# Optimization experiments

Hardware: AMD Instinct MI355X
Metric: run time of the kernel (lower is better)

Reference implementation:

```python
import jax, jax.numpy as jnp
from jax import lax
import numpy as np
from functools import reduce

# --- module hyperparameters (init_kwargs defaults) ---
T_LOW = 0.5; T_HIGH = 0.9; SIGMAS = (1.0, 2.0); BETA = 0.5
Z_RADIUS = 1; XY_RADIUS = 0; DUST_MIN_SIZE = 100; EPS = 1e-7
MAX_HYST_ITERS = 256   # flood-fill iteration cap (converges far earlier on real data)
MAX_CC_ITERS = 256     # label-propagation iteration cap


def _gauss_kernel(sigma):
    # separable gaussian, truncate at 3 sigma (standard scipy convention)
    r = int(3.0 * sigma + 0.5)
    x = np.arange(-r, r + 1, dtype=np.float32)
    k = np.exp(-(x * x) / (2.0 * sigma * sigma))
    return jnp.asarray(k / k.sum())


def _conv1d_axis(v, k, axis):
    # 'same' zero-padded 1D correlation along `axis` of a 3D volume
    r = k.shape[0] // 2
    pad = [(0, 0)] * 3; pad[axis] = (r, r)
    vp = jnp.pad(v, pad)
    n = v.shape[axis]
    out = jnp.zeros_like(v)
    for i in range(k.shape[0]):  # tiny fixed tap loop, vectorized over the volume
        sl = [slice(None)] * 3; sl[axis] = slice(i, i + n)
        out = out + k[i] * vp[tuple(sl)]
    return out


def _shifts6(x, pad_val):
    # 6-connected neighbor views (cross connectivity, matches ndi default)
    p = jnp.pad(x, 1, constant_values=pad_val)
    c = slice(1, -1)
    return (p[:-2, c, c], p[2:, c, c], p[c, :-2, c], p[c, 2:, c], p[c, c, :-2], p[c, c, 2:])


def _axis_morph(m, axis, radius, dilate):
    # box dilation/erosion along one axis (box SE is separable)
    op = jnp.logical_or if dilate else jnp.logical_and
    pad_val = (not dilate)
    for _ in range(radius):
        pad = [(1, 1) if a == axis else (0, 0) for a in range(3)]
        p = jnp.pad(m, pad, constant_values=pad_val)
        lo = tuple(slice(0, -2) if a == axis else slice(None) for a in range(3))
        hi = tuple(slice(2, None) if a == axis else slice(None) for a in range(3))
        m = op(op(m, p[lo]), p[hi])
    return m


def _hysteresis(vol):
    # keep low-threshold voxels connected to a high-threshold voxel (flood fill)
    low = vol > T_LOW
    high = vol > T_HIGH
    def body(st):
        m, _, i = st
        nm = m
        for s in _shifts6(m, False):
            nm = nm | s
        nm = nm & low
        return nm, jnp.any(nm != m), i + 1
    mask, _, _ = lax.while_loop(lambda st: st[1] & (st[2] < MAX_HYST_ITERS), body,
                                (high, jnp.bool_(True), jnp.int32(0)))
    return mask


def _closing(mask):
    # anisotropic binary closing with box SE (2*z_r+1, 2*xy_r+1, 2*xy_r+1)
    for axis, r in ((0, Z_RADIUS), (1, XY_RADIUS), (2, XY_RADIUS)):
        mask = _axis_morph(mask, axis, r, dilate=True)
    for axis, r in ((0, Z_RADIUS), (1, XY_RADIUS), (2, XY_RADIUS)):
        mask = _axis_morph(mask, axis, r, dilate=False)
    return mask


def _remove_small(mask):
    # connected-component labeling via max-label propagation, then size filter
    n = mask.size
    idx = jnp.arange(1, n + 1, dtype=jnp.int32).reshape(mask.shape)
    lab0 = jnp.where(mask, idx, 0)
    def body(st):
        l, _, i = st
        nl = l
        for s in _shifts6(l, 0):
            nl = jnp.maximum(nl, s)
        nl = jnp.where(mask, nl, 0)
        return nl, jnp.any(nl != l), i + 1
    lab, _, _ = lax.while_loop(lambda st: st[1] & (st[2] < MAX_CC_ITERS), body,
                               (lab0, jnp.bool_(True), jnp.int32(0)))
    counts = jax.ops.segment_sum(mask.ravel().astype(jnp.int32), lab.ravel(), num_segments=n + 1)
    return mask & (counts[lab] >= DUST_MIN_SIZE)


def _process_volume(v):
    d2 = jnp.asarray([1.0, -2.0, 1.0], v.dtype)
    surfs = []
    for sigma in SIGMAS:
        k = _gauss_kernel(sigma)
        s = v
        for ax in range(3):
            s = _conv1d_axis(s, k, ax)
        scale = sigma * sigma
        fxx = _conv1d_axis(s, d2, 0) * scale
        fyy = _conv1d_axis(s, d2, 1) * scale
        fzz = _conv1d_axis(s, d2, 2) * scale
        surf = jnp.exp(-(fxx * fxx + fyy * fyy) / (BETA * BETA * (fzz * fzz + EPS))) * jnp.abs(fzz)
        mx = surf.max()
        surfs.append(jnp.where(mx > 0, surf / (mx + EPS), jnp.zeros_like(surf)))
    surfaceness = reduce(jnp.maximum, surfs)  # max over sigma stack
    vol = lax.stop_gradient(v * surfaceness)  # binarization pipeline is piecewise constant
    mask = _hysteresis(vol)
    mask = _closing(mask)
    if DUST_MIN_SIZE > 0:
        mask = _remove_small(mask)
    return mask.astype(v.dtype)


def setup_inputs() -> dict:
    key = jax.random.key(0)
    outputs = jax.random.uniform(key, (2, 192, 192, 192), dtype=jnp.float32)
    return {"outputs": outputs}


def reference(outputs):
    return jax.vmap(_process_volume)(outputs)
```

## Files before the change

kernel.cpp:

```cpp
#include <hip/hip_runtime.h>
#include <cmath>

#define D3   192
#define SZP  (D3*D3)
#define NVOX (D3*D3*D3)
#define NTOT (2*NVOX)
#define NBLK (NTOT/256)
#define W3   (NTOT/64)
#define WBLK (W3/256)
#define NSUM (W3/64)
#define NQ   (NTOT/4)
#define NQB  (NQ/256)
#define BPB  (NVOX/256)

#define HT 16
#define HH 8
#define HL (HT+2*HH)
#define HLDS (HL*HL*3)
#define NHT  (12*12*2)

typedef unsigned long long u64;

struct Taps13 { float k[13]; };

__device__ __forceinline__ void coords(int idx, int& x, int& y, int& z, int& b) {
  x = idx % D3;
  y = (idx / D3) % D3;
  z = (idx / SZP) % D3;
  b = idx / NVOX;
}

template<int AXIS, int R>
__global__ void __launch_bounds__(256) conv1d_k(const float* __restrict__ in,
                                                float* __restrict__ out, Taps13 t) {
  int idx = blockIdx.x * 256 + threadIdx.x;
  int x, y, z, b; coords(idx, x, y, z, b);
  int c = (AXIS == 0) ? z : (AXIS == 1) ? y : x;
  const int stride = (AXIS == 0) ? SZP : (AXIS == 1) ? D3 : 1;
  float acc = 0.f;
#pragma unroll
  for (int i = -R; i <= R; ++i) {
    int cc = c + i;
    if (cc >= 0 && cc < D3)
      acc = __fadd_rn(acc, __fmul_rn(t.k[i + R], in[idx + i * stride]));
  }
  out[idx] = acc;
}

__global__ void __launch_bounds__(256) surf_k(const float* __restrict__ s,
                                              float* __restrict__ surf,
                                              float* __restrict__ bmax,
                                              float scale) {
  int idx = blockIdx.x * 256 + threadIdx.x;
  int x, y, z, b; coords(idx, x, y, z, b);
  float ctr = s[idx];
  float fxx, fyy, fzz;
  { float acc = 0.f;
    if (z > 0)      acc = __fadd_rn(acc, __fmul_rn(1.f, s[idx - SZP]));
    acc = __fadd_rn(acc, __fmul_rn(-2.f, ctr));
    if (z < D3 - 1) acc = __fadd_rn(acc, __fmul_rn(1.f, s[idx + SZP]));
    fxx = __fmul_rn(acc, scale); }
  { float acc = 0.f;
    if (y > 0)      acc = __fadd_rn(acc, __fmul_rn(1.f, s[idx - D3]));
    acc = __fadd_rn(acc, __fmul_rn(-2.f, ctr));
    if (y < D3 - 1) acc = __fadd_rn(acc, __fmul_rn(1.f, s[idx + D3]));
    fyy = __fmul_rn(acc, scale); }
  { float acc = 0.f;
    if (x > 0)      acc = __fadd_rn(acc, __fmul_rn(1.f, s[idx - 1]));
    acc = __fadd_rn(acc, __fmul_rn(-2.f, ctr));
    if (x < D3 - 1) acc = __fadd_rn(acc, __fmul_rn(1.f, s[idx + 1]));
    fzz = __fmul_rn(acc, scale); }

  float num = __fadd_rn(__fmul_rn(fxx, fxx), __fmul_rn(fyy, fyy));
  float den = __fmul_rn(0.25f, __fadd_rn(__fmul_rn(fzz, fzz), 1e-7f));
  float arg = __fdiv_rn(-num, den);
  float sv  = __fmul_rn(expf(arg), fabsf(fzz));
  surf[idx] = sv;

  float m = sv;
  #pragma unroll
  for (int off = 32; off > 0; off >>= 1) m = fmaxf(m, __shfl_down(m, off));
  __shared__ float wred[4];
  int lane = threadIdx.x & 63, wid = threadIdx.x >> 6;
  if (lane == 0) wred[wid] = m;
  __syncthreads();
  if (threadIdx.x == 0)
    bmax[blockIdx.x] = fmaxf(fmaxf(wred[0], wred[1]), fmaxf(wred[2], wred[3]));
}

__global__ void __launch_bounds__(256) reduce_max_k(const float* __restrict__ bmax,
                                                    unsigned int* __restrict__ mxp) {
  int b = blockIdx.x;
  const float* p = bmax + b * BPB;
  float m = 0.f;
  for (int i = threadIdx.x; i < BPB; i += 256) m = fmaxf(m, p[i]);
  #pragma unroll
  for (int off = 32; off > 0; off >>= 1) m = fmaxf(m, __shfl_down(m, off));
  __shared__ float wred[4];
  int lane = threadIdx.x & 63, wid = threadIdx.x >> 6;
  if (lane == 0) wred[wid] = m;
  __syncthreads();
  if (threadIdx.x == 0)
    mxp[b] = __float_as_uint(fmaxf(fmaxf(wred[0], wred[1]), fmaxf(wred[2], wred[3])));
}

__global__ void __launch_bounds__(256) mask_init_pack_k(const float* __restrict__ v,
                                                        const float* __restrict__ s1,
                                                        const float* __restrict__ s2,
                                                        const unsigned int* __restrict__ mx,
                                                        u64* __restrict__ lowW,
                                                        u64* __restrict__ mW) {
  int idx = blockIdx.x * 256 + threadIdx.x;
  int b = idx / NVOX;
  float m1 = __uint_as_float(mx[b]);
  float m2 = __uint_as_float(mx[2 + b]);
  float n1 = (m1 > 0.f) ? __fdiv_rn(s1[idx], __fadd_rn(m1, 1e-7f)) : 0.f;
  float n2 = (m2 > 0.f) ? __fdiv_rn(s2[idx], __fadd_rn(m2, 1e-7f)) : 0.f;
  float vol = __fmul_rn(v[idx], fmaxf(n1, n2));
  u64 bl = __ballot(vol > 0.5f);
  u64 bh = __ballot(vol > 0.9f);
  if ((threadIdx.x & 63) == 0) {
    lowW[idx >> 6] = bl;
    mW[idx >> 6]   = bh;
  }
}

__global__ void __launch_bounds__(256) hyst8_k(const u64* __restrict__ src,
                                               u64* __restrict__ dst,
                                               const u64* __restrict__ lowW,
                                               const int* __restrict__ fprev,
                                               int* __restrict__ fcur,
                                               int* __restrict__ chg, int iter) {
  if (iter > 0 && chg[iter - 1] == 0) return;
  const int r = blockIdx.x + 12 * blockIdx.y + 144 * blockIdx.z;
  if (iter > 0) {
    bool act = false;
    for (int dz = -1; dz <= 1 && !act; ++dz) {
      int zz = (int)blockIdx.y + dz; if (zz < 0 || zz >= 12) continue;
      for (int dy = -1; dy <= 1; ++dy) {
        int yy = (int)blockIdx.x + dy; if (yy < 0 || yy >= 12) continue;
        if (fprev[yy + 12 * zz + 144 * blockIdx.z]) { act = true; break; }
      }
    }
    if (!act) { if (threadIdx.x == 0) fcur[r] = 0; return; }
  }

  __shared__ u64 sA[HLDS], sB[HLDS];
  __shared__ int blkC;
  const int t = threadIdx.x;
  if (t == 0) blkC = 0;
  const int y0 = blockIdx.x * HT - HH;
  const int z0 = blockIdx.y * HT - HH;
  const int b  = blockIdx.z;

  u64 lowr[4][3], orig[4][3];
#pragma unroll
  for (int j = 0; j < 4; ++j) {
    int l = t + 256 * j;
    int yy = l & 31, zz = l >> 5;
    int y = y0 + yy, z = z0 + zz;
    bool in = (y >= 0 && y < D3 && z >= 0 && z < D3);
    int wb = 3 * y + 576 * z + 110592 * b;
#pragma unroll
    for (int xw = 0; xw < 3; ++xw) {
      u64 sv = in ? src[wb + xw]  : 0ull;
      u64 lv = in ? lowW[wb + xw] : 0ull;
      sA[l * 3 + xw] = sv;
      orig[j][xw] = sv;
      lowr[j][xw] = lv;
    }
  }
  __syncthreads();

  u64* cur = sA; u64* nxt = sB;
  for (int s = 0; s < 8; ++s) {
#pragma unroll
    for (int j = 0; j < 4; ++j) {
      int l = t + 256 * j;
      int yy = l & 31, zz = l >> 5;
      int base = l * 3;
      u64 w0 = cur[base], w1 = cur[base + 1], w2 = cur[base + 2];
      u64 n0 = w0 | (w0 << 1) | (w0 >> 1) | (w1 << 63);
      u64 n1 = w1 | (w1 << 1) | (w1 >> 1) | (w0 >> 63) | (w2 << 63);
      u64 n2 = w2 | (w2 << 1) | (w2 >> 1) | (w1 >> 63);
      if (yy > 0)  { n0 |= cur[base - 3];  n1 |= cur[base - 2];  n2 |= cur[base - 1]; }
      if (yy < 31) { n0 |= cur[base + 3];  n1 |= cur[base + 4];  n2 |= cur[base + 5]; }
      if (zz > 0)  { n0 |= cur[base - 96]; n1 |= cur[base - 95]; n2 |= cur[base - 94]; }
      if (zz < 31) { n0 |= cur[base + 96]; n1 |= cur[base + 97]; n2 |= cur[base + 98]; }
      nxt[base]     = n0 & lowr[j][0];
      nxt[base + 1] = n1 & lowr[j][1];
      nxt[base + 2] = n2 & lowr[j][2];
    }
    __syncthreads();
    u64* tmp = cur; cur = nxt; nxt = tmp;
  }

  bool ch = false;
#pragma unroll
  for (int j = 0; j < 4; ++j) {
    int l = t + 256 * j;
    int yy = l & 31, zz = l >> 5;
    if (yy >= HH && yy < HH + HT && zz >= HH && zz < HH + HT) {
      int y = y0 + yy, z = z0 + zz;
      int wb = 3 * y + 576 * z + 110592 * b;
#pragma unroll
      for (int xw = 0; xw < 3; ++xw) {
        u64 o = cur[l * 3 + xw];
        ch |= (o != orig[j][xw]);
        dst[wb + xw] = o;
      }
    }
  }
  if (ch) blkC = 1;
  __syncthreads();
  if (t == 0) { fcur[r] = blkC; if (blkC) chg[iter] = 1; }
}

__global__ void __launch_bounds__(256) close_z_k(const u64* __restrict__ mi,
                                                 u64* __restrict__ mo) {
  int w = blockIdx.x * 256 + threadIdx.x;
  int z = (w / 576) % D3;
  u64 c   = mi[w];
  u64 zm1 = (z > 0)      ? mi[w - 576]  : 0ull;
  u64 zm2 = (z > 1)      ? mi[w - 1152] : 0ull;
  u64 zp1 = (z < D3 - 1) ? mi[w + 576]  : 0ull;
  u64 zp2 = (z < D3 - 2) ? mi[w + 1152] : 0ull;
  u64 d0 = c | zm1 | zp1;
  u64 e  = d0;
  if (z > 0)      e &= (zm2 | zm1 | c);
  if (z < D3 - 1) e &= (c | zp1 | zp2);
  mo[w] = e;
}

__global__ void __launch_bounds__(256) label_init_k(const u64* __restrict__ closedW,
                                                    int* __restrict__ lab) {
  int idx = blockIdx.x * 256 + threadIdx.x;
  int bit = (int)((closedW[idx >> 6] >> (idx & 63)) & 1ull);
  lab[idx] = bit ? (idx % NVOX) + 1 : 0;
}

__device__ __forceinline__ int imax2(int a, int b) { return a > b ? a : b; }

__global__ void __launch_bounds__(256) cc_word_k(const int* __restrict__ src,
                                                 int* __restrict__ dst,
                                                 const u64* __restrict__ chgPrev,
                                                 u64* __restrict__ chgCur,
                                                 const u64* __restrict__ sumPrev,
                                                 u64* __restrict__ sumCur,
                                                 const u64* __restrict__ closedW,
                                                 int* __restrict__ chg, int iter) {
  if (iter > 0 && chg[iter - 1] == 0) return;
  __shared__ int blkC;
  if (threadIdx.x == 0) blkC = 0;
  __syncthreads();

  const int w = blockIdx.x * 256 + threadIdx.x;
  const int xw = w % 3;
  const int y  = (w / 3) % D3;
  const int z  = (w / 576) % D3;

  u64 F, U;
  if (iter == 0) {
    F = ~0ull; U = 0ull;
  } else {
    u64 c  = ((sumPrev[w >> 6] >> (w & 63)) & 1ull) ? chgPrev[w] : 0ull;
    u64 cl = 0ull, cr = 0ull, ym = 0ull, yp = 0ull, zm = 0ull, zp = 0ull;
    if (xw > 0      && ((sumPrev[(w - 1) >> 6]   >> ((w - 1) & 63))   & 1ull)) cl = chgPrev[w - 1];
    if (xw < 2      && ((sumPrev[(w + 1) >> 6]   >> ((w + 1) & 63))   & 1ull)) cr = chgPrev[w + 1];
    if (y > 0       && ((sumPrev[(w - 3) >> 6]   >> ((w - 3) & 63))   & 1ull)) ym = chgPrev[w - 3];
    if (y < D3 - 1  && ((sumPrev[(w + 3) >> 6]   >> ((w + 3) & 63))   & 1ull)) yp = chgPrev[w + 3];
    if (z > 0       && ((sumPrev[(w - 576) >> 6] >> ((w - 576) & 63)) & 1ull)) zm = chgPrev[w - 576];
    if (z < D3 - 1  && ((sumPrev[(w + 576) >> 6] >> ((w + 576) & 63)) & 1ull)) zp = chgPrev[w + 576];
    u64 nb = (c << 1) | (c >> 1) | (cl >> 63) | (cr << 63) | ym | yp | zm | zp;
    if ((nb | c) == 0ull) { F = 0ull; U = 0ull; }
    else {
      u64 cw = closedW[w];
      F = nb & cw;
      U = c & cw & ~F;
    }
  }

  u64 P = F | U;
  u64 newc = 0;
  if (P) {
    int idx0 = xw * 64 + D3 * y + SZP * z + (w / 110592) * NVOX;
#pragma unroll
    for (int q = 0; q < 16; ++q) {
      if (!((P >> (4 * q)) & 0xFull)) continue;
      int idx = idx0 + 4 * q;
      int4 s = *(const int4*)(src + idx);
      int4 o = s;
      if ((F >> (4 * q)) & 0xFull) {
        int x = xw * 64 + 4 * q;
        const int4 z4 = make_int4(0, 0, 0, 0);
        int4 yv = (y > 0)      ? *(const int4*)(src + idx - D3)  : z4;
        int4 yw = (y < D3 - 1) ? *(const int4*)(src + idx + D3)  : z4;
        int4 zv = (z > 0)      ? *(const int4*)(src + idx - SZP) : z4;
        int4 zw = (z < D3 - 1) ? *(const int4*)(src + idx + SZP) : z4;
        int lf = (x > 0)       ? src[idx - 1] : 0;
        int rt = (x < D3 - 4)  ? src[idx + 4] : 0;
        o.x = s.x ? imax2(imax2(imax2(s.x, lf),  imax2(s.y, yv.x)), imax2(imax2(yw.x, zv.x), zw.x)) : 0;
        o.y = s.y ? imax2(imax2(imax2(s.y, s.x), imax2(s.z, yv.y)), imax2(imax2(yw.y, zv.y), zw.y)) : 0;
        o.z = s.z ? imax2(imax2(imax2(s.z, s.y), imax2(s.w, yv.z)), imax2(imax2(yw.z, zv.z), zw.z)) : 0;
        o.w = s.w ? imax2(imax2(imax2(s.w, s.z), imax2(rt,  yv.w)), imax2(imax2(yw.w, zv.w), zw.w)) : 0;
      }
      *(int4*)(dst + idx) = o;
      u64 df = (u64)((o.x != s.x) | ((o.y != s.y) << 1) |
                     ((o.z != s.z) << 2) | ((o.w != s.w) << 3));
      newc |= df << (4 * q);
    }
  }

  u64 bal = __ballot(newc != 0ull);
  if (newc) chgCur[w] = newc;
  if ((threadIdx.x & 63) == 0) sumCur[w >> 6] = bal;
  if (bal) blkC = 1;
  __syncthreads();
  if (threadIdx.x == 0 && blkC) chg[iter] = 1;
}

__global__ void __launch_bounds__(256) count_k(const int* __restrict__ lab,
                                               unsigned int* __restrict__ counts) {
  int q = blockIdx.x * 256 + threadIdx.x;
  int idx = q << 2;
  int b = idx / NVOX;
  int4 L = *(const int4*)(lab + idx);
  unsigned int* cb = counts + b * NVOX;
  if (L.x > 0) atomicAdd(&cb[L.x - 1], 1u);
  if (L.y > 0) atomicAdd(&cb[L.y - 1], 1u);
  if (L.z > 0) atomicAdd(&cb[L.z - 1], 1u);
  if (L.w > 0) atomicAdd(&cb[L.w - 1], 1u);
}

__global__ void __launch_bounds__(256) final_k(const int* __restrict__ lab,
                                               const unsigned int* __restrict__ counts,
                                               float* __restrict__ out) {
  int q = blockIdx.x * 256 + threadIdx.x;
  int idx = q << 2;
  int b = idx / NVOX;
  int4 L = *(const int4*)(lab + idx);
  const unsigned int* cb = counts + b * NVOX;
  float4 rr;
  rr.x = (L.x > 0 && cb[L.x - 1] >= 100u) ? 1.f : 0.f;
  rr.y = (L.y > 0 && cb[L.y - 1] >= 100u) ? 1.f : 0.f;
  rr.z = (L.z > 0 && cb[L.z - 1] >= 100u) ? 1.f : 0.f;
  rr.w = (L.w > 0 && cb[L.w - 1] >= 100u) ? 1.f : 0.f;
  *(float4*)(out + idx) = rr;
}

static float np_sum_f32(const float* a, int n) {
  if (n < 8) { float res = 0.f; for (int i = 0; i < n; i++) res += a[i]; return res; }
  float r[8]; for (int j = 0; j < 8; j++) r[j] = a[j];
  int i = 8;
  for (; i < n - (n % 8); i += 8) for (int j = 0; j < 8; j++) r[j] += a[i + j];
  float res = ((r[0] + r[1]) + (r[2] + r[3])) + ((r[4] + r[5]) + (r[6] + r[7]));
  for (; i < n; i++) res += a[i];
  return res;
}

extern "C" void kernel_launch(void* const* d_in, const int* in_sizes, int n_in,
                              void* d_out, int out_size, void* d_ws, size_t ws_size,
                              hipStream_t stream) {
  const float* v = (const float*)d_in[0];
  float* out = (float*)d_out;
  char* base = (char*)d_ws;
  const size_t SZBUF = (size_t)NTOT * 4;
  const size_t SZW   = (size_t)W3 * 8;

  float* A  = (float*)base;
  float* Cf = (float*)(base + SZBUF);
  unsigned int* mx = (unsigned int*)(base + 2 * SZBUF);
  float* bmax = (float*)(base + 2 * SZBUF + 256);
  float* Bf = (float*)d_out;

  u64* lowW    = (u64*)base;
  u64* mWA     = (u64*)(base + SZW);
  u64* mWB     = (u64*)(base + 2 * SZW);
  u64* closedW = (u64*)(base + 3 * SZW);
  u64* chgWA   = (u64*)(base + 4 * SZW);
  u64* chgWB   = (u64*)(base + 5 * SZW);
  u64* sumA    = (u64*)(base + 6 * SZW);
  u64* sumB    = sumA + NSUM;
  int* chgH = (int*)(sumB + NSUM);
  int* chgC = chgH + 32;
  int* hF0  = chgC + 256;
  int* hF1  = hF0 + NHT;

  int* labA = (int*)Bf;
  int* labB = (int*)Cf;
  unsigned int* counts = (unsigned int*)Cf;

  dim3 g(NBLK), gw(WBLK), gq(NQB), blk(256);

  const double sigmas[2] = {1.0, 2.0};
  for (int si = 0; si < 2; ++si) {
    double sigma = sigmas[si];
    int r = (int)(3.0 * sigma + 0.5);
    int n = 2 * r + 1;
    float a[13], k[13];
    for (int i = 0; i < n; i++) {
      float xx = (float)(i - r);
      float t  = xx * xx;
      float arg = -(t) / (float)(2.0 * sigma * sigma);
      a[i] = (float)std::exp((double)arg);
    }
    float ssum = np_sum_f32(a, n);
    for (int i = 0; i < n; i++) k[i] = a[i] / ssum;

    Taps13 T = {};
    for (int i = 0; i < n; i++) T.k[i] = k[i];
    float scale = (float)(sigma * sigma);
    float* starget = (si == 0) ? Cf : Bf;

    if (r == 3) {
      conv1d_k<0, 3><<<g, blk, 0, stream>>>(v,  A,  T);
      conv1d_k<1, 3><<<g, blk, 0, stream>>>(A,  Bf, T);
      conv1d_k<2, 3><<<g, blk, 0, stream>>>(Bf, A,  T);
    } else {
      conv1d_k<0, 6><<<g, blk, 0, stream>>>(v,  A,  T);
      conv1d_k<1, 6><<<g, blk, 0, stream>>>(A,  Bf, T);
      conv1d_k<2, 6><<<g, blk, 0, stream>>>(Bf, A,  T);
    }
    surf_k<<<g, blk, 0, stream>>>(A, starget, bmax, scale);
    reduce_max_k<<<dim3(2), blk, 0, stream>>>(bmax, mx + 2 * si);
  }

  hipMemsetAsync(chgH, 0, (32 + 256) * 4, stream);
  mask_init_pack_k<<<g, blk, 0, stream>>>(v, Cf, Bf, mx, lowW, mWA);

  for (int it = 0; it < 32; ++it) {
    const u64* s = (it & 1) ? mWB : mWA;
    u64*       d = (it & 1) ? mWA : mWB;
    const int* fp = (it & 1) ? hF0 : hF1;
    int*       fc = (it & 1) ? hF1 : hF0;
    hyst8_k<<<dim3(12, 12, 2), blk, 0, stream>>>(s, d, lowW, fp, fc, chgH, it);
  }

  close_z_k<<<gw, blk, 0, stream>>>(mWA, closedW);

  label_init_k<<<g, blk, 0, stream>>>(closedW, labA);
  for (int it = 0; it < 256; ++it) {
    const int* s = (it & 1) ? labB : labA;
    int*       d = (it & 1) ? labA : labB;
    const u64* cp = (it & 1) ? chgWB : chgWA;
    u64*       cc = (it & 1) ? chgWA : chgWB;
    const u64* sp = (it & 1) ? sumB : sumA;
    u64*       sc = (it & 1) ? sumA : sumB;
    cc_word_k<<<gw, blk, 0, stream>>>(s, d, cp, cc, sp, sc, closedW, chgC, it);
  }

  hipMemsetAsync(counts, 0, SZBUF, stream);
  count_k<<<gq, blk, 0, stream>>>(labA, counts);
  final_k<<<gq, blk, 0, stream>>>(labA, counts, out);
}
```

Baseline: 1.867 ms.

## Fuse label init with first propagation pass and skip empty words in count/final

Replaces the separate label-init kernel and the first full-volume label propagation iteration with a single word-parallel kernel. It writes both label buffers directly, computing the first max-propagation step analytically from the closed mask bits, and seeds the change bitmaps. The count and final kernels now check the packed mask and skip label and count reads for empty voxel groups. This cuts one full dense pass plus label reads in sparse regions, at the cost of a more intricate init that must exactly match one propagation step. The memset of the control area is also widened to cover the hysteresis flag buffers.

```diff
diff --git a/kernel.cpp b/kernel.cpp
--- a/kernel.cpp
+++ b/kernel.cpp
@@ -232,11 +232,53 @@
   mo[w] = e;
 }
 
-__global__ void __launch_bounds__(256) label_init_k(const u64* __restrict__ closedW,
-                                                    int* __restrict__ lab) {
-  int idx = blockIdx.x * 256 + threadIdx.x;
-  int bit = (int)((closedW[idx >> 6] >> (idx & 63)) & 1ull);
-  lab[idx] = bit ? (idx % NVOX) + 1 : 0;
+__global__ void __launch_bounds__(256) cc_init_fused_k(const u64* __restrict__ closedW,
+                                                       int* __restrict__ lab0,
+                                                       int* __restrict__ lab1,
+                                                       u64* __restrict__ chgW,
+                                                       u64* __restrict__ sumW,
+                                                       int* __restrict__ chg) {
+  __shared__ int blkC;
+  if (threadIdx.x == 0) blkC = 0;
+  __syncthreads();
+  const int w = blockIdx.x * 256 + threadIdx.x;
+  const int xw = w % 3;
+  const int y  = (w / 3) % D3;
+  const int z  = (w / 576) % D3;
+  u64 cw = closedW[w];
+  u64 xp = cw >> 1;
+  if (xw < 2) xp |= (closedW[w + 1] & 1ull) << 63;
+  u64 yp = (y < D3 - 1) ? closedW[w + 3]   : 0ull;
+  u64 zp = (z < D3 - 1) ? closedW[w + 576] : 0ull;
+  u64 newc = cw & (xp | yp | zp);
+
+  const int rel0  = xw * 64 + D3 * y + SZP * z;
+  const int vbase = rel0 + (w / 110592) * NVOX;
+#pragma unroll
+  for (int q = 0; q < 16; ++q) {
+    int sh = 4 * q;
+    unsigned nib = (unsigned)((cw >> sh) & 0xFull);
+    int4 s0 = make_int4(0, 0, 0, 0), s1 = make_int4(0, 0, 0, 0);
+    if (nib) {
+      unsigned nxp = (unsigned)((xp >> sh) & 0xFull);
+      unsigned nyp = (unsigned)((yp >> sh) & 0xFull);
+      unsigned nzp = (unsigned)((zp >> sh) & 0xFull);
+      int L0 = rel0 + sh + 1;
+      if (nib & 1u) { s0.x = L0;     s1.x = L0     + ((nzp & 1u) ? SZP : (nyp & 1u) ? D3 : (nxp & 1u) ? 1 : 0); }
+      if (nib & 2u) { s0.y = L0 + 1; s1.y = L0 + 1 + ((nzp & 2u) ? SZP : (nyp & 2u) ? D3 : (nxp & 2u) ? 1 : 0); }
+      if (nib & 4u) { s0.z = L0 + 2; s1.z = L0 + 2 + ((nzp & 4u) ? SZP : (nyp & 4u) ? D3 : (nxp & 4u) ? 1 : 0); }
+      if (nib & 8u) { s0.w = L0 + 3; s1.w = L0 + 3 + ((nzp & 8u) ? SZP : (nyp & 8u) ? D3 : (nxp & 8u) ? 1 : 0); }
+    }
+    *(int4*)(lab0 + vbase + sh) = s0;
+    *(int4*)(lab1 + vbase + sh) = s1;
+  }
+
+  u64 bal = __ballot(newc != 0ull);
+  if (newc) chgW[w] = newc;
+  if ((threadIdx.x & 63) == 0) sumW[w >> 6] = bal;
+  if (bal) blkC = 1;
+  __syncthreads();
+  if (threadIdx.x == 0 && blkC) chg[0] = 1;
 }
 
 __device__ __forceinline__ int imax2(int a, int b) { return a > b ? a : b; }
@@ -260,9 +302,7 @@
   const int z  = (w / 576) % D3;
 
   u64 F, U;
-  if (iter == 0) {
-    F = ~0ull; U = 0ull;
-  } else {
+  {
     u64 c  = ((sumPrev[w >> 6] >> (w & 63)) & 1ull) ? chgPrev[w] : 0ull;
     u64 cl = 0ull, cr = 0ull, ym = 0ull, yp = 0ull, zm = 0ull, zp = 0ull;
     if (xw > 0      && ((sumPrev[(w - 1) >> 6]   >> ((w - 1) & 63))   & 1ull)) cl = chgPrev[w - 1];
@@ -320,12 +360,16 @@
 }
 
 __global__ void __launch_bounds__(256) count_k(const int* __restrict__ lab,
+                                               const u64* __restrict__ closedW,
                                                unsigned int* __restrict__ counts) {
   int q = blockIdx.x * 256 + threadIdx.x;
   int idx = q << 2;
+  u64 cw = closedW[idx >> 6];
+  unsigned nib = (unsigned)((cw >> (idx & 63)) & 0xFull);
+  if (!nib) return;
   int b = idx / NVOX;
   int4 L = *(const int4*)(lab + idx);
-  unsigned int* cb = counts + b * NVOX;
+  unsigned int* cb = counts + (size_t)b * NVOX;
   if (L.x > 0) atomicAdd(&cb[L.x - 1], 1u);
   if (L.y > 0) atomicAdd(&cb[L.y - 1], 1u);
   if (L.z > 0) atomicAdd(&cb[L.z - 1], 1u);
@@ -333,18 +377,23 @@
 }
 
 __global__ void __launch_bounds__(256) final_k(const int* __restrict__ lab,
+                                               const u64* __restrict__ closedW,
                                                const unsigned int* __restrict__ counts,
                                                float* __restrict__ out) {
   int q = blockIdx.x * 256 + threadIdx.x;
   int idx = q << 2;
-  int b = idx / NVOX;
-  int4 L = *(const int4*)(lab + idx);
-  const unsigned int* cb = counts + b * NVOX;
-  float4 rr;
-  rr.x = (L.x > 0 && cb[L.x - 1] >= 100u) ? 1.f : 0.f;
-  rr.y = (L.y > 0 && cb[L.y - 1] >= 100u) ? 1.f : 0.f;
-  rr.z = (L.z > 0 && cb[L.z - 1] >= 100u) ? 1.f : 0.f;
-  rr.w = (L.w > 0 && cb[L.w - 1] >= 100u) ? 1.f : 0.f;
+  u64 cw = closedW[idx >> 6];
+  unsigned nib = (unsigned)((cw >> (idx & 63)) & 0xFull);
+  float4 rr = make_float4(0.f, 0.f, 0.f, 0.f);
+  if (nib) {
+    int b = idx / NVOX;
+    int4 L = *(const int4*)(lab + idx);
+    const unsigned int* cb = counts + (size_t)b * NVOX;
+    rr.x = (L.x > 0 && cb[L.x - 1] >= 100u) ? 1.f : 0.f;
+    rr.y = (L.y > 0 && cb[L.y - 1] >= 100u) ? 1.f : 0.f;
+    rr.z = (L.z > 0 && cb[L.z - 1] >= 100u) ? 1.f : 0.f;
+    rr.w = (L.w > 0 && cb[L.w - 1] >= 100u) ? 1.f : 0.f;
+  }
   *(float4*)(out + idx) = rr;
 }
 
@@ -385,6 +434,7 @@
   int* chgC = chgH + 32;
   int* hF0  = chgC + 256;
   int* hF1  = hF0 + NHT;
+  size_t ctrlBytes = (char*)(hF1 + NHT) - (char*)chgH;
 
   int* labA = (int*)Bf;
   int* labB = (int*)Cf;
@@ -425,7 +475,7 @@
     reduce_max_k<<<dim3(2), blk, 0, stream>>>(bmax, mx + 2 * si);
   }
 
-  hipMemsetAsync(chgH, 0, (32 + 256) * 4, stream);
+  hipMemsetAsync(chgH, 0, ctrlBytes, stream);
   mask_init_pack_k<<<g, blk, 0, stream>>>(v, Cf, Bf, mx, lowW, mWA);
 
   for (int it = 0; it < 32; ++it) {
@@ -438,8 +488,9 @@
 
   close_z_k<<<gw, blk, 0, stream>>>(mWA, closedW);
 
-  label_init_k<<<g, blk, 0, stream>>>(closedW, labA);
-  for (int it = 0; it < 256; ++it) {
+  cc_init_fused_k<<<gw, blk, 0, stream>>>(closedW, labA, labB, chgWB, sumB, chgC);
+
+  for (int it = 1; it < 256; ++it) {
     const int* s = (it & 1) ? labB : labA;
     int*       d = (it & 1) ? labA : labB;
     const u64* cp = (it & 1) ? chgWB : chgWA;
@@ -450,6 +501,6 @@
   }
 
   hipMemsetAsync(counts, 0, SZBUF, stream);
-  count_k<<<gq, blk, 0, stream>>>(labA, counts);
-  final_k<<<gq, blk, 0, stream>>>(labA, counts, out);
-}
+  count_k<<<gq, blk, 0, stream>>>(labA, closedW, counts);
+  final_k<<<gq, blk, 0, stream>>>(labA, closedW, counts, out);
+}
```

Result: faster. 1.620 ms (median of 2 runs) (-13.2%).
